# Kernel tuning notes

Measured on AMD Instinct MI355X. Metric: run time of the kernel, lower is better.

The kernel has to match this reference:

```python
import jax, jax.numpy as jnp
import numpy as np

B, S, D, H = 4, 2048, 2048, 16
Dh = D // H
BASE = 10000.0


def _rope_tables(seq_len, head_dim, dtype=jnp.float32):
    inv_freq = 1.0 / (BASE ** (jnp.arange(0, head_dim, 2, dtype=jnp.float32) / head_dim))
    t = jnp.arange(seq_len, dtype=jnp.float32)
    freqs = jnp.outer(t, inv_freq)              # [S, Dh/2]
    emb = jnp.concatenate([freqs, freqs], -1)   # [S, Dh]
    return jnp.cos(emb).astype(dtype), jnp.sin(emb).astype(dtype)


def _rotate_half(x):
    d = x.shape[-1] // 2
    return jnp.concatenate([-x[..., d:], x[..., :d]], axis=-1)


def setup_inputs() -> dict:
    key = jax.random.key(0)
    ks = jax.random.split(key, 5)
    std = D ** -0.5
    x = jax.random.normal(ks[0], (B, S, D), jnp.float32)
    Wq = jax.random.normal(ks[1], (D, D), jnp.float32) * std
    Wk = jax.random.normal(ks[2], (D, D), jnp.float32) * std
    Wv = jax.random.normal(ks[3], (D, D), jnp.float32) * std
    Wo = jax.random.normal(ks[4], (D, D), jnp.float32) * std
    attn_mask = jnp.triu(jnp.ones((S, S), dtype=bool), k=1)  # True = masked (causal)
    return {"x": x, "attn_mask": attn_mask, "Wq": Wq, "Wk": Wk, "Wv": Wv, "Wo": Wo}


def reference(x, attn_mask, Wq, Wk, Wv, Wo):
    b, s, d = x.shape
    # projections (nn.Linear: x @ W.T), split heads -> [B, H, S, Dh]
    q = (x @ Wq.T).reshape(b, s, H, Dh).transpose(0, 2, 1, 3)
    k = (x @ Wk.T).reshape(b, s, H, Dh).transpose(0, 2, 1, 3)
    v = (x @ Wv.T).reshape(b, s, H, Dh).transpose(0, 2, 1, 3)
    cos, sin = _rope_tables(s, Dh, x.dtype)     # [S, Dh]
    q = q * cos + _rotate_half(q) * sin
    k = k * cos + _rotate_half(k) * sin
    scale = Dh ** -0.5
    scores = jnp.einsum('bhqd,bhkd->bhqk', q, k) * scale
    scores = jnp.where(attn_mask[None, None, :, :], -jnp.inf, scores)
    weights = jax.nn.softmax(scores, axis=-1)
    out = jnp.einsum('bhqk,bhkd->bhqd', weights, v)
    out = out.transpose(0, 2, 1, 3).reshape(b, s, d)
    return out @ Wo.T
```

## Files before the change

kernel.cpp:

```cpp
#include <hip/hip_runtime.h>
#include <cstdint>
#include <cmath>

#define NB 4
#define NS 2048
#define ND 2048
#define NH 16
#define NDH 128
#define NM (NB*NS)

typedef unsigned short u16;
typedef __bf16 bf16x8 __attribute__((ext_vector_type(8)));
typedef u16    u16x8  __attribute__((ext_vector_type(8)));
typedef u16    u16x4  __attribute__((ext_vector_type(4)));
typedef float  f32x4  __attribute__((ext_vector_type(4)));
typedef float  f32x16 __attribute__((ext_vector_type(16)));
typedef unsigned u32x4_t __attribute__((ext_vector_type(4)));

__device__ __forceinline__ u16 f2bf(float f) {
  unsigned u = __float_as_uint(f);
  u += 0x7fffu + ((u >> 16) & 1u);
  return (u16)(u >> 16);
}
__device__ __forceinline__ float bf2f(u16 h) {
  return __uint_as_float(((unsigned)h) << 16);
}
__device__ __forceinline__ void gld16(const void* g, void* l) {
  __builtin_amdgcn_global_load_lds((__attribute__((address_space(1))) void*)g,
                                   (__attribute__((address_space(3))) void*)l,
                                   16, 0, 0);
}
__device__ __forceinline__ f32x4 mfma_bf16(bf16x8 a, bf16x8 b, f32x4 c) {
  return __builtin_amdgcn_mfma_f32_16x16x32_bf16(a, b, c, 0, 0, 0);
}
__device__ __forceinline__ f32x16 mfma32_bf16(bf16x8 a, bf16x8 b, f32x16 c) {
  return __builtin_amdgcn_mfma_f32_32x32x16_bf16(a, b, c, 0, 0, 0);
}
__device__ __forceinline__ unsigned cvtpk(float lo, float hi) {
  unsigned r;
  asm("v_cvt_pk_bf16_f32 %0, %1, %2" : "=v"(r) : "v"(lo), "v"(hi));
  return r;
}
__device__ __forceinline__ void p32swap(unsigned &a, unsigned &b) {
  asm volatile("v_permlane32_swap_b32 %0, %1" : "+v"(a), "+v"(b));
}

__global__ void cvt_bf16_kernel(const float* __restrict__ in, u16* __restrict__ out, int n8) {
  int i = blockIdx.x * 256 + threadIdx.x;
  if (i >= n8) return;
  const float4* p = (const float4*)in + (size_t)i * 2;
  float4 a = p[0], b = p[1];
  u16x8 r;
  r[0]=f2bf(a.x); r[1]=f2bf(a.y); r[2]=f2bf(a.z); r[3]=f2bf(a.w);
  r[4]=f2bf(b.x); r[5]=f2bf(b.y); r[6]=f2bf(b.z); r[7]=f2bf(b.w);
  ((u16x8*)out)[i] = r;
}

__global__ void cvt4_bf16_kernel(const float* __restrict__ i0, const float* __restrict__ i1,
                                 const float* __restrict__ i2, const float* __restrict__ i3,
                                 u16* o0, u16* o1, u16* o2, u16* o3, int n8each) {
  int idx = blockIdx.x * 256 + threadIdx.x;
  int w = idx / n8each, i = idx - w * n8each;
  if (w >= 4) return;
  const float* in = (w == 0) ? i0 : (w == 1) ? i1 : (w == 2) ? i2 : i3;
  u16* out = (w == 0) ? o0 : (w == 1) ? o1 : (w == 2) ? o2 : o3;
  const float4* p = (const float4*)in + (size_t)i * 2;
  float4 a = p[0], b = p[1];
  u16x8 r;
  r[0]=f2bf(a.x); r[1]=f2bf(a.y); r[2]=f2bf(a.z); r[3]=f2bf(a.w);
  r[4]=f2bf(b.x); r[5]=f2bf(b.y); r[6]=f2bf(b.z); r[7]=f2bf(b.w);
  ((u16x8*)out)[i] = r;
}

__global__ void rope_tables_kernel(float* __restrict__ cosT, float* __restrict__ sinT) {
  int s = blockIdx.x, d = threadIdx.x;
  double inv = pow(10000.0, -(double)d / 64.0);
  float ang = (float)((double)s * inv);
  cosT[s*64 + d] = cosf(ang);
  sinT[s*64 + d] = sinf(ang);
}

__global__ void rope_apply_kernel(u16* __restrict__ Qb, u16* __restrict__ Kb,
                                  const float* __restrict__ cosT,
                                  const float* __restrict__ sinT, int nthr) {
  int gidx = blockIdx.x * 256 + threadIdx.x;
  u16* X = (gidx < nthr) ? Qb : Kb;
  int idx = (gidx < nthr) ? gidx : gidx - nthr;
  int pc = idx & 7, h = (idx >> 3) & (NH - 1), m = idx >> 7;
  int s = m & (NS - 1);
  int d0 = pc * 8;
  size_t base = (size_t)m * ND + h * NDH + d0;
  u16x8 v0 = *(const u16x8*)(X + base);
  u16x8 v1 = *(const u16x8*)(X + base + 64);
  u16x8 r0, r1;
#pragma unroll
  for (int j = 0; j < 8; ++j) {
    float c  = cosT[s*64 + d0 + j];
    float sn = sinT[s*64 + d0 + j];
    float x0 = bf2f(v0[j]), x1 = bf2f(v1[j]);
    r0[j] = f2bf(x0 * c - x1 * sn);
    r1[j] = f2bf(x1 * c + x0 * sn);
  }
  *(u16x8*)(X + base)      = r0;
  *(u16x8*)(X + base + 64) = r1;
}

#define BARX do { __builtin_amdgcn_s_barrier(); __builtin_amdgcn_sched_barrier(0); } while (0)
#define VM4  do { asm volatile("s_waitcnt vmcnt(4)" ::: "memory"); \
                  __builtin_amdgcn_sched_barrier(0); } while (0)
#define GP(BUF, KS, MH, LOADB, WAITV, DOBAR, STAGE) do {                          \
  bf16x8 af[4];                                                                   \
  _Pragma("unroll")                                                               \
  for (int mf = 0; mf < 4; ++mf)                                                  \
    af[mf] = *(const bf16x8*)(Asb + (BUF)*32768 + (KS)*16384 + arow + ((MH)*4+mf)*1024); \
  if (LOADB) {                                                                    \
    _Pragma("unroll")                                                             \
    for (int nf = 0; nf < 4; ++nf)                                                \
      bfr[nf] = *(const bf16x8*)(Bsb + (BUF)*32768 + (KS)*16384 + brow + nf*1024); \
  }                                                                               \
  STAGE;                                                                          \
  __builtin_amdgcn_s_setprio(1);                                                  \
  _Pragma("unroll")                                                               \
  for (int mf = 0; mf < 4; ++mf)                                                  \
    _Pragma("unroll")                                                             \
    for (int nf = 0; nf < 4; ++nf)                                                \
      acc[(MH)*4+mf][nf] = mfma_bf16(af[mf], bfr[nf], acc[(MH)*4+mf][nf]);        \
  __builtin_amdgcn_s_setprio(0);                                                  \
  if (WAITV) VM4;                                                                 \
  if (DOBAR) BARX;                                                                \
} while (0)

template <typename OutT>
__global__ __launch_bounds__(512, 2) void gemm256_kernel(
    const u16* __restrict__ A,
    const u16* __restrict__ B0, const u16* __restrict__ B1, const u16* __restrict__ B2,
    OutT* __restrict__ C0, OutT* __restrict__ C1, OutT* __restrict__ C2,
    int Nd, int Kd) {
  __shared__ __align__(16) char Asb[65536];
  __shared__ __align__(16) char Bsb[65536];
  int tid = threadIdx.x;
  int wave = tid >> 6, lane = tid & 63;
  int li = lane & 15, lg = lane >> 4;
  int wr = wave >> 2, wc = wave & 3;
  int w  = (int)blockIdx.x >> 8;
  int tb = (int)blockIdx.x & 255;
  const u16* Bw = (w == 0) ? B0 : (w == 1) ? B1 : B2;
  OutT*      C  = (w == 0) ? C0 : (w == 1) ? C1 : C2;
  int NTn = Nd >> 8;
  int swz = (tb & 7) * 32 + (tb >> 3);
  int m0 = (swz / NTn) << 8, n0 = (swz % NTn) << 8;

  int rswz = (lg * 16) ^ (((li >> 1) & 3) << 4);
  int arow = (wr * 128 + li) * 64 + rswz;
  int brow = (wc *  64 + li) * 64 + rswz;

  int srow = wave * 16 + (lane >> 2);
  int scswz = ((lane & 3) * 16) ^ (((srow >> 1) & 3) << 4);
  size_t rowB = (size_t)Kd * 2;
  const char* Asrc = (const char*)A  + (size_t)(m0 + srow) * rowB + scswz;
  const char* Bsrc = (const char*)Bw + (size_t)(n0 + srow) * rowB + scswz;
  char* Adst = Asb + wave * 1024;
  char* Bdst = Bsb + wave * 1024;
  size_t half2 = rowB << 7;

  auto stageA = [&](int buf, int ks, int tile) {
    const char* s = Asrc + (size_t)tile * 128 + ks * 64;
    char* d = Adst + buf * 32768 + ks * 16384;
    gld16(s, d);
    gld16(s + half2, d + 8192);
  };
  auto stageB = [&](int buf, int ks, int tile) {
    const char* s = Bsrc + (size_t)tile * 128 + ks * 64;
    char* d = Bdst + buf * 32768 + ks * 16384;
    gld16(s, d);
    gld16(s + half2, d + 8192);
  };

  f32x4 acc[8][4] = {};
  bf16x8 bfr[4];

  int NKT = Kd >> 6;
  int NIT = NKT >> 1;

  stageA(0, 0, 0); stageA(0, 1, 0); stageB(0, 0, 0); stageB(0, 1, 0);
  stageA(1, 0, 1); stageB(1, 0, 1);
  asm volatile("s_waitcnt vmcnt(4)" ::: "memory");
  __builtin_amdgcn_sched_barrier(0);
  BARX;

  for (int j = 0; j < NIT; ++j) {
    int t1  = 2*j + 1;
    int tn0 = (2*j + 2) & (NKT - 1);
    int tn1 = (2*j + 3) & (NKT - 1);
    GP(0, 0, 0, true,  false, false, { stageA(1, 1, t1);  });
    GP(0, 0, 1, false, false, true,  { stageB(1, 1, t1);  });
    GP(0, 1, 1, true,  false, false, { stageA(0, 0, tn0); });
    GP(0, 1, 0, false, true,  true,  { stageB(0, 0, tn0); });
    GP(1, 0, 0, true,  false, false, { stageA(0, 1, tn0); });
    GP(1, 0, 1, false, false, true,  { stageB(0, 1, tn0); });
    GP(1, 1, 1, true,  false, false, { stageA(1, 0, tn1); });
    GP(1, 1, 0, false, true,  true,  { stageB(1, 0, tn1); });
  }
  asm volatile("s_waitcnt vmcnt(0)" ::: "memory");

  int rbase = m0 + wr*128 + lg*4;
  int cbase = n0 + wc*64 + li;
#pragma unroll
  for (int am = 0; am < 8; ++am)
#pragma unroll
    for (int nf = 0; nf < 4; ++nf)
#pragma unroll
      for (int r = 0; r < 4; ++r) {
        size_t off = (size_t)(rbase + am*16 + r) * Nd + (cbase + nf*16);
        if constexpr (sizeof(OutT) == 2) C[off] = f2bf(acc[am][nf][r]);
        else                             C[off] = acc[am][nf][r];
      }
}

__global__ __launch_bounds__(512, 2) void flash_attn_kernel(
    const u16* __restrict__ Q, const u16* __restrict__ K, const u16* __restrict__ V,
    u16* __restrict__ O) {
  __shared__ __align__(16) u16 Ks[2*64*128];
  __shared__ __align__(16) u16 Vt[2*128*64];
  int tid = threadIdx.x, wv = tid >> 6, lane = tid & 63;
  int ql = lane & 31, hi = lane >> 5;
  int b = blockIdx.x >> 4, h = blockIdx.x & 15;
  int qt = (int)gridDim.y - 1 - (int)blockIdx.y;
  int q0 = qt << 8;
  int qw = q0 + wv*32;
  int qa = qw + ql;
  int swzl = (ql & 7) << 4;
  int vswz = ((ql >> 1) & 7) << 4;
  const float qscale = 0.08838834764831845f * 1.4426950408889634f;

  bf16x8 qf[8];
  {
    const u16* qp = Q + (size_t)(b*NS + qa) * ND + h*NDH + hi*8;
#pragma unroll
    for (int ds = 0; ds < 8; ++ds) {
      u16x8 t = *(const u16x8*)(qp + ds*16);
      u16x8 r;
#pragma unroll
      for (int j = 0; j < 8; ++j) r[j] = f2bf(bf2f(t[j]) * qscale);
      qf[ds] = *(bf16x8*)&r;
    }
  }
  f32x16 o0 = {}, o1 = {}, o2 = {}, o3 = {};
  float m_run = -INFINITY, l_run = 0.f;

  const char* Kg = (const char*)(K + (size_t)b*NS*ND + h*NDH);
  const char* Vg = (const char*)(V + (size_t)b*NS*ND + h*NDH);
  const int ROWB = ND * 2;

  int p   = tid & 31;
  int kvg = tid >> 5;

  auto issueKV = [&](int kv0, int buf, unsigned (&dlo)[4], unsigned (&dhi)[4]) {
    const char* vrow = Vg + (size_t)(kv0 + kvg*4) * ROWB;
#pragma unroll
    for (int j = 0; j < 4; ++j) {
      dlo[j] = *(const unsigned*)(vrow + j*ROWB + p*4);
      dhi[j] = *(const unsigned*)(vrow + j*ROWB + 128 + p*4);
    }
    char* ksb = (char*)Ks + buf*16384;
#pragma unroll
    for (int c = 0; c < 2; ++c) {
      int s = c*8192 + wv*1024 + lane*16;
      int row = s >> 8;
      int within = (s & 255) ^ ((row & 7) << 4);
      gld16(Kg + (size_t)(kv0 + row)*ROWB + within, ksb + c*8192 + wv*1024);
    }
    __builtin_amdgcn_sched_barrier(0);
  };

  auto dostep = [&](int kv0, int buf, const unsigned (&dlo)[4], const unsigned (&dhi)[4],
                    bool hasNext) {
    if (hasNext) asm volatile("s_waitcnt vmcnt(10)" ::: "memory");
    else         asm volatile("s_waitcnt vmcnt(0)"  ::: "memory");
    __builtin_amdgcn_sched_barrier(0);
    __builtin_amdgcn_s_barrier();
    __builtin_amdgcn_sched_barrier(0);

    char* vtb = (char*)Vt + buf*16384;
    const char* ksb = (const char*)Ks + buf*16384;

    {
      u16x4 rA, rB, rC, rD;
#pragma unroll
      for (int j = 0; j < 4; ++j) {
        rA[j] = (u16)dlo[j]; rB[j] = (u16)(dlo[j] >> 16);
        rC[j] = (u16)dhi[j]; rD[j] = (u16)(dhi[j] >> 16);
      }
      int ws = (p & 7) << 4;
      int a0 = ((2*p   )*128 + kvg*8) ^ ws;
      int a1 = ((2*p+ 1)*128 + kvg*8) ^ ws;
      int a2 = ((2*p+64)*128 + kvg*8) ^ ws;
      int a3 = ((2*p+65)*128 + kvg*8) ^ ws;
      *(u16x4*)(vtb + a0) = rA;
      *(u16x4*)(vtb + a1) = rB;
      *(u16x4*)(vtb + a2) = rC;
      *(u16x4*)(vtb + a3) = rD;
    }

    f32x16 p0 = {}, p1 = {};
    __builtin_amdgcn_s_setprio(1);
#pragma unroll
    for (int ds = 0; ds < 8; ++ds) {
      bf16x8 kf0 = *(const bf16x8*)(ksb + ((ql*256 + ds*32 + hi*16) ^ swzl));
      p0 = mfma32_bf16(kf0, qf[ds], p0);
      bf16x8 kf1 = *(const bf16x8*)(ksb + (((32+ql)*256 + ds*32 + hi*16) ^ swzl));
      p1 = mfma32_bf16(kf1, qf[ds], p1);
    }
    __builtin_amdgcn_s_setprio(0);

    if (kv0 + 63 > qw) {
      int thresh = qa - kv0 - 4*hi;
#pragma unroll
      for (int r = 0; r < 16; ++r) {
        int c0 = (r & 3) + 8*(r >> 2);
        p0[r] = (c0      > thresh) ? -INFINITY : p0[r];
        p1[r] = (c0 + 32 > thresh) ? -INFINITY : p1[r];
      }
    }

    float mx[16];
#pragma unroll
    for (int r = 0; r < 16; ++r) mx[r] = fmaxf(p0[r], p1[r]);
#pragma unroll
    for (int s = 8; s > 0; s >>= 1)
#pragma unroll
      for (int r = 0; r < 8; ++r) if (r < s) mx[r] = fmaxf(mx[r], mx[r + s]);
    float pmax = fmaxf(mx[0], __shfl_xor(mx[0], 32, 64));

    if (!__all(pmax <= m_run + 8.f)) {
      float mn = fmaxf(m_run, pmax);
      float corr = __builtin_amdgcn_exp2f(m_run - mn);
      m_run = mn; l_run *= corr;
#pragma unroll
      for (int r = 0; r < 16; ++r) {
        float cw = __shfl(corr, (r & 3) + 8*(r >> 2) + 4*hi, 64);
        o0[r] *= cw; o1[r] *= cw; o2[r] *= cw; o3[r] *= cw;
      }
    }

    float sm[16];
#pragma unroll
    for (int r = 0; r < 16; ++r) {
      p0[r] = __builtin_amdgcn_exp2f(p0[r] - m_run);
      p1[r] = __builtin_amdgcn_exp2f(p1[r] - m_run);
      sm[r] = p0[r] + p1[r];
    }
#pragma unroll
    for (int s = 8; s > 0; s >>= 1)
#pragma unroll
      for (int r = 0; r < 8; ++r) if (r < s) sm[r] += sm[r + s];
    l_run += sm[0] + __shfl_xor(sm[0], 32, 64);

    bf16x8 pa0, pa1, pa2, pa3;
#define MKPA(P, B, OUT) {                              \
      unsigned a0 = cvtpk(P[(B)+0], P[(B)+1]);         \
      unsigned b0 = cvtpk(P[(B)+4], P[(B)+5]);         \
      p32swap(a0, b0);                                 \
      unsigned a1 = cvtpk(P[(B)+2], P[(B)+3]);         \
      unsigned b1 = cvtpk(P[(B)+6], P[(B)+7]);         \
      p32swap(a1, b1);                                 \
      u32x4_t w; w[0]=a0; w[1]=a1; w[2]=b0; w[3]=b1;   \
      OUT = *(bf16x8*)&w; }
    MKPA(p0, 0, pa0)
    MKPA(p0, 8, pa1)
    MKPA(p1, 0, pa2)
    MKPA(p1, 8, pa3)
#undef MKPA

    asm volatile("s_waitcnt lgkmcnt(0)" ::: "memory");
    __builtin_amdgcn_sched_barrier(0);
    __builtin_amdgcn_s_barrier();
    __builtin_amdgcn_sched_barrier(0);

    __builtin_amdgcn_s_setprio(1);
#define PVT(OT, T) {                                                        \
      _Pragma("unroll")                                                     \
      for (int ks = 0; ks < 4; ++ks) {                                      \
        int a = ((((T)*32 + ql)*128 + ks*32 + hi*16) ^ vswz);               \
        bf16x8 vf = *(const bf16x8*)(vtb + a);                              \
        OT = mfma32_bf16(ks==0?pa0:ks==1?pa1:ks==2?pa2:pa3, vf, OT);        \
      } }
    PVT(o0, 0)
    PVT(o1, 1)
    PVT(o2, 2)
    PVT(o3, 3)
#undef PVT
    __builtin_amdgcn_s_setprio(0);
  };

  int nt = 4*qt + 4;
  unsigned dloA[4], dhiA[4], dloB[4], dhiB[4];
  issueKV(0, 0, dloA, dhiA);
  for (int t = 0; ; t += 2) {
    bool h1 = (t+1 < nt);
    if (h1) issueKV((t+1)*64, 1, dloB, dhiB);
    dostep(t*64, 0, dloA, dhiA, h1);
    if (!h1) break;
    bool h2 = (t+2 < nt);
    if (h2) issueKV((t+2)*64, 0, dloA, dhiA);
    dostep((t+1)*64, 1, dloB, dhiB, h2);
    if (!h2) break;
  }

  float inv = 1.0f / l_run;
#pragma unroll
  for (int r = 0; r < 16; ++r) {
    int crow = (r & 3) + 8*(r >> 2) + 4*hi;
    float iv = __shfl(inv, crow, 64);
    size_t base = (size_t)(b*NS + qw + crow) * ND + h*NDH + ql;
    O[base +  0] = f2bf(o0[r] * iv);
    O[base + 32] = f2bf(o1[r] * iv);
    O[base + 64] = f2bf(o2[r] * iv);
    O[base + 96] = f2bf(o3[r] * iv);
  }
}

extern "C" void kernel_launch(void* const* d_in, const int* in_sizes, int n_in,
                              void* d_out, int out_size, void* d_ws, size_t ws_size,
                              hipStream_t stream) {
  const float* x  = (const float*)d_in[0];
  const float* Wq = (const float*)d_in[2];
  const float* Wk = (const float*)d_in[3];
  const float* Wv = (const float*)d_in[4];
  const float* Wo = (const float*)d_in[5];

  char* ws = (char*)d_ws;
  const size_t SZ_MD = (size_t)NM * ND * 2;
  const size_t SZ_W  = (size_t)ND * ND * 2;
  u16* xb  = (u16*)(ws);
  u16* Qb  = (u16*)(ws + SZ_MD);
  u16* Kb  = (u16*)(ws + 2*SZ_MD);
  u16* Vb  = (u16*)(ws + 3*SZ_MD);
  u16* Ab  = (u16*)(ws + 4*SZ_MD);
  u16* Wqb = (u16*)(ws + 5*SZ_MD);
  u16* Wkb = (u16*)(ws + 5*SZ_MD + SZ_W);
  u16* Wvb = (u16*)(ws + 5*SZ_MD + 2*SZ_W);
  u16* Wob = (u16*)(ws + 5*SZ_MD + 3*SZ_W);
  float* cosT = (float*)(ws + 5*SZ_MD + 4*SZ_W);
  float* sinT = (float*)(ws + 5*SZ_MD + 4*SZ_W + (size_t)NS*64*4);
  size_t needed = 5*SZ_MD + 4*SZ_W + 2*(size_t)NS*64*4;
  if (ws_size < needed) return;

  {
    int n8 = (NM * ND) / 8;
    cvt_bf16_kernel<<<(n8 + 255)/256, 256, 0, stream>>>(x, xb, n8);
    int w8 = (ND * ND) / 8;
    cvt4_bf16_kernel<<<(4*w8 + 255)/256, 256, 0, stream>>>(Wq, Wk, Wv, Wo,
                                                           Wqb, Wkb, Wvb, Wob, w8);
  }
  rope_tables_kernel<<<NS, 64, 0, stream>>>(cosT, sinT);

  gemm256_kernel<u16><<<3*256, 512, 0, stream>>>(xb, Wqb, Wkb, Wvb,
                                                 Qb, Kb, Vb, ND, ND);

  {
    int nthr = NM * NH * 8;
    rope_apply_kernel<<<(2*nthr)/256, 256, 0, stream>>>(Qb, Kb, cosT, sinT, nthr);
  }

  flash_attn_kernel<<<dim3(NB*NH, NS/256), 512, 0, stream>>>(Qb, Kb, Vb, Ab);

  gemm256_kernel<float><<<256, 512, 0, stream>>>(Ab, Wob, nullptr, nullptr,
                                                 (float*)d_out, nullptr, nullptr, ND, ND);
}
```

Baseline: 413.4 us.

## Pair long and short causal query tiles per block to share K/V loads

Each flash-attention block now handles two query tiles, a late one (4+y) and an early one (3-y), so every block does the same amount of causal work. Each K/V tile staged in LDS is used by both query sets. The grid shrinks from 8 to 4 tiles along y. This is meant to remove causal load imbalance and halve K/V traffic, but it doubles the accumulator and Q-fragment registers, which risks spilling or lower occupancy under launch_bounds(512,2), and halves the block count.

```diff
diff --git a/kernel.cpp b/kernel.cpp
--- a/kernel.cpp
+++ b/kernel.cpp
@@ -44,6 +44,16 @@
 __device__ __forceinline__ void p32swap(unsigned &a, unsigned &b) {
   asm volatile("v_permlane32_swap_b32 %0, %1" : "+v"(a), "+v"(b));
 }
+
+#define MKPA(P, B, OUT) {                              \
+      unsigned a0 = cvtpk(P[(B)+0], P[(B)+1]);         \
+      unsigned b0 = cvtpk(P[(B)+4], P[(B)+5]);         \
+      p32swap(a0, b0);                                 \
+      unsigned a1 = cvtpk(P[(B)+2], P[(B)+3]);         \
+      unsigned b1 = cvtpk(P[(B)+6], P[(B)+7]);         \
+      p32swap(a1, b1);                                 \
+      u32x4_t w_; w_[0]=a0; w_[1]=a1; w_[2]=b0; w_[3]=b1; \
+      OUT = *(bf16x8*)&w_; }
 
 __global__ void cvt_bf16_kernel(const float* __restrict__ in, u16* __restrict__ out, int n8) {
   int i = blockIdx.x * 256 + threadIdx.x;
@@ -217,6 +227,79 @@
       }
 }
 
+#define QKSM(SUF) do {                                                         \
+    f32x16 p0 = {}, p1 = {};                                                   \
+    __builtin_amdgcn_s_setprio(1);                                             \
+    _Pragma("unroll")                                                          \
+    for (int ds = 0; ds < 8; ++ds) {                                           \
+      bf16x8 kf0 = *(const bf16x8*)(ksb + ((ql*256 + ds*32 + hi*16) ^ swzl));  \
+      p0 = mfma32_bf16(kf0, qf##SUF[ds], p0);                                  \
+      bf16x8 kf1 = *(const bf16x8*)(ksb + (((32+ql)*256 + ds*32 + hi*16) ^ swzl)); \
+      p1 = mfma32_bf16(kf1, qf##SUF[ds], p1);                                  \
+    }                                                                          \
+    __builtin_amdgcn_s_setprio(0);                                             \
+    if (kv0 + 63 > qw##SUF) {                                                  \
+      int thresh = qa##SUF - kv0 - 4*hi;                                       \
+      _Pragma("unroll")                                                        \
+      for (int r = 0; r < 16; ++r) {                                           \
+        int c0 = (r & 3) + 8*(r >> 2);                                         \
+        p0[r] = (c0      > thresh) ? -INFINITY : p0[r];                        \
+        p1[r] = (c0 + 32 > thresh) ? -INFINITY : p1[r];                        \
+      }                                                                        \
+    }                                                                          \
+    float mx[16];                                                              \
+    _Pragma("unroll")                                                          \
+    for (int r = 0; r < 16; ++r) mx[r] = fmaxf(p0[r], p1[r]);                  \
+    _Pragma("unroll")                                                          \
+    for (int s_ = 8; s_ > 0; s_ >>= 1)                                         \
+      _Pragma("unroll")                                                        \
+      for (int r = 0; r < 8; ++r) if (r < s_) mx[r] = fmaxf(mx[r], mx[r + s_]); \
+    float pmax = fmaxf(mx[0], __shfl_xor(mx[0], 32, 64));                      \
+    if (!__all(pmax <= m##SUF + 8.f)) {                                        \
+      float mn = fmaxf(m##SUF, pmax);                                          \
+      float corr = __builtin_amdgcn_exp2f(m##SUF - mn);                        \
+      m##SUF = mn; l##SUF *= corr;                                             \
+      _Pragma("unroll")                                                        \
+      for (int r = 0; r < 16; ++r) {                                           \
+        float cw = __shfl(corr, (r & 3) + 8*(r >> 2) + 4*hi, 64);              \
+        o##SUF##0[r] *= cw; o##SUF##1[r] *= cw;                                \
+        o##SUF##2[r] *= cw; o##SUF##3[r] *= cw;                                \
+      }                                                                        \
+    }                                                                          \
+    float sm[16];                                                              \
+    _Pragma("unroll")                                                          \
+    for (int r = 0; r < 16; ++r) {                                             \
+      p0[r] = __builtin_amdgcn_exp2f(p0[r] - m##SUF);                          \
+      p1[r] = __builtin_amdgcn_exp2f(p1[r] - m##SUF);                          \
+      sm[r] = p0[r] + p1[r];                                                   \
+    }                                                                          \
+    _Pragma("unroll")                                                          \
+    for (int s_ = 8; s_ > 0; s_ >>= 1)                                         \
+      _Pragma("unroll")                                                        \
+      for (int r = 0; r < 8; ++r) if (r < s_) sm[r] += sm[r + s_];             \
+    l##SUF += sm[0] + __shfl_xor(sm[0], 32, 64);                               \
+    MKPA(p0, 0, pa##SUF##0)                                                    \
+    MKPA(p0, 8, pa##SUF##1)                                                    \
+    MKPA(p1, 0, pa##SUF##2)                                                    \
+    MKPA(p1, 8, pa##SUF##3)                                                    \
+  } while (0)
+
+#define PVT1(OT, T, P0, P1, P2, P3)                                            \
+    _Pragma("unroll")                                                          \
+    for (int ks_ = 0; ks_ < 4; ++ks_) {                                        \
+      int a_ = ((((T)*32 + ql)*128 + ks_*32 + hi*16) ^ vswz);                  \
+      bf16x8 vf = *(const bf16x8*)(vtb + a_);                                  \
+      OT = mfma32_bf16(ks_==0?P0:ks_==1?P1:ks_==2?P2:P3, vf, OT);              \
+    }
+#define PVS(SUF) do {                                                          \
+    __builtin_amdgcn_s_setprio(1);                                             \
+    PVT1(o##SUF##0, 0, pa##SUF##0, pa##SUF##1, pa##SUF##2, pa##SUF##3)         \
+    PVT1(o##SUF##1, 1, pa##SUF##0, pa##SUF##1, pa##SUF##2, pa##SUF##3)         \
+    PVT1(o##SUF##2, 2, pa##SUF##0, pa##SUF##1, pa##SUF##2, pa##SUF##3)         \
+    PVT1(o##SUF##3, 3, pa##SUF##0, pa##SUF##1, pa##SUF##2, pa##SUF##3)         \
+    __builtin_amdgcn_s_setprio(0);                                             \
+  } while (0)
+
 __global__ __launch_bounds__(512, 2) void flash_attn_kernel(
     const u16* __restrict__ Q, const u16* __restrict__ K, const u16* __restrict__ V,
     u16* __restrict__ O) {
@@ -225,28 +308,37 @@
   int tid = threadIdx.x, wv = tid >> 6, lane = tid & 63;
   int ql = lane & 31, hi = lane >> 5;
   int b = blockIdx.x >> 4, h = blockIdx.x & 15;
-  int qt = (int)gridDim.y - 1 - (int)blockIdx.y;
-  int q0 = qt << 8;
-  int qw = q0 + wv*32;
-  int qa = qw + ql;
+  int y = blockIdx.y;
+  int qtA = 4 + y, qtB = 3 - y;
+  int q0A = qtA << 8, q0B = qtB << 8;
+  int qwA = q0A + wv*32, qwB = q0B + wv*32;
+  int qaA = qwA + ql,  qaB = qwB + ql;
   int swzl = (ql & 7) << 4;
   int vswz = ((ql >> 1) & 7) << 4;
   const float qscale = 0.08838834764831845f * 1.4426950408889634f;
 
-  bf16x8 qf[8];
+  bf16x8 qfA[8], qfB[8];
   {
-    const u16* qp = Q + (size_t)(b*NS + qa) * ND + h*NDH + hi*8;
+    const u16* qpA = Q + (size_t)(b*NS + qaA) * ND + h*NDH + hi*8;
+    const u16* qpB = Q + (size_t)(b*NS + qaB) * ND + h*NDH + hi*8;
 #pragma unroll
     for (int ds = 0; ds < 8; ++ds) {
-      u16x8 t = *(const u16x8*)(qp + ds*16);
-      u16x8 r;
-#pragma unroll
-      for (int j = 0; j < 8; ++j) r[j] = f2bf(bf2f(t[j]) * qscale);
-      qf[ds] = *(bf16x8*)&r;
+      u16x8 tA = *(const u16x8*)(qpA + ds*16);
+      u16x8 tB = *(const u16x8*)(qpB + ds*16);
+      u16x8 rA, rB;
+#pragma unroll
+      for (int j = 0; j < 8; ++j) {
+        rA[j] = f2bf(bf2f(tA[j]) * qscale);
+        rB[j] = f2bf(bf2f(tB[j]) * qscale);
+      }
+      qfA[ds] = *(bf16x8*)&rA;
+      qfB[ds] = *(bf16x8*)&rB;
     }
   }
-  f32x16 o0 = {}, o1 = {}, o2 = {}, o3 = {};
-  float m_run = -INFINITY, l_run = 0.f;
+  f32x16 oA0 = {}, oA1 = {}, oA2 = {}, oA3 = {};
+  f32x16 oB0 = {}, oB1 = {}, oB2 = {}, oB3 = {};
+  float mA = -INFINITY, lA = 0.f, mB = -INFINITY, lB = 0.f;
+  bf16x8 paA0, paA1, paA2, paA3, paB0, paB1, paB2, paB3;
 
   const char* Kg = (const char*)(K + (size_t)b*NS*ND + h*NDH);
   const char* Vg = (const char*)(V + (size_t)b*NS*ND + h*NDH);
@@ -292,131 +384,55 @@
         rC[j] = (u16)dhi[j]; rD[j] = (u16)(dhi[j] >> 16);
       }
       int ws = (p & 7) << 4;
-      int a0 = ((2*p   )*128 + kvg*8) ^ ws;
-      int a1 = ((2*p+ 1)*128 + kvg*8) ^ ws;
-      int a2 = ((2*p+64)*128 + kvg*8) ^ ws;
-      int a3 = ((2*p+65)*128 + kvg*8) ^ ws;
-      *(u16x4*)(vtb + a0) = rA;
-      *(u16x4*)(vtb + a1) = rB;
-      *(u16x4*)(vtb + a2) = rC;
-      *(u16x4*)(vtb + a3) = rD;
+      *(u16x4*)(vtb + (((2*p   )*128 + kvg*8) ^ ws)) = rA;
+      *(u16x4*)(vtb + (((2*p+ 1)*128 + kvg*8) ^ ws)) = rB;
+      *(u16x4*)(vtb + (((2*p+64)*128 + kvg*8) ^ ws)) = rC;
+      *(u16x4*)(vtb + (((2*p+65)*128 + kvg*8) ^ ws)) = rD;
     }
 
-    f32x16 p0 = {}, p1 = {};
-    __builtin_amdgcn_s_setprio(1);
-#pragma unroll
-    for (int ds = 0; ds < 8; ++ds) {
-      bf16x8 kf0 = *(const bf16x8*)(ksb + ((ql*256 + ds*32 + hi*16) ^ swzl));
-      p0 = mfma32_bf16(kf0, qf[ds], p0);
-      bf16x8 kf1 = *(const bf16x8*)(ksb + (((32+ql)*256 + ds*32 + hi*16) ^ swzl));
-      p1 = mfma32_bf16(kf1, qf[ds], p1);
-    }
-    __builtin_amdgcn_s_setprio(0);
-
-    if (kv0 + 63 > qw) {
-      int thresh = qa - kv0 - 4*hi;
-#pragma unroll
-      for (int r = 0; r < 16; ++r) {
-        int c0 = (r & 3) + 8*(r >> 2);
-        p0[r] = (c0      > thresh) ? -INFINITY : p0[r];
-        p1[r] = (c0 + 32 > thresh) ? -INFINITY : p1[r];
-      }
-    }
-
-    float mx[16];
-#pragma unroll
-    for (int r = 0; r < 16; ++r) mx[r] = fmaxf(p0[r], p1[r]);
-#pragma unroll
-    for (int s = 8; s > 0; s >>= 1)
-#pragma unroll
-      for (int r = 0; r < 8; ++r) if (r < s) mx[r] = fmaxf(mx[r], mx[r + s]);
-    float pmax = fmaxf(mx[0], __shfl_xor(mx[0], 32, 64));
-
-    if (!__all(pmax <= m_run + 8.f)) {
-      float mn = fmaxf(m_run, pmax);
-      float corr = __builtin_amdgcn_exp2f(m_run - mn);
-      m_run = mn; l_run *= corr;
-#pragma unroll
-      for (int r = 0; r < 16; ++r) {
-        float cw = __shfl(corr, (r & 3) + 8*(r >> 2) + 4*hi, 64);
-        o0[r] *= cw; o1[r] *= cw; o2[r] *= cw; o3[r] *= cw;
-      }
-    }
-
-    float sm[16];
-#pragma unroll
-    for (int r = 0; r < 16; ++r) {
-      p0[r] = __builtin_amdgcn_exp2f(p0[r] - m_run);
-      p1[r] = __builtin_amdgcn_exp2f(p1[r] - m_run);
-      sm[r] = p0[r] + p1[r];
-    }
-#pragma unroll
-    for (int s = 8; s > 0; s >>= 1)
-#pragma unroll
-      for (int r = 0; r < 8; ++r) if (r < s) sm[r] += sm[r + s];
-    l_run += sm[0] + __shfl_xor(sm[0], 32, 64);
-
-    bf16x8 pa0, pa1, pa2, pa3;
-#define MKPA(P, B, OUT) {                              \
-      unsigned a0 = cvtpk(P[(B)+0], P[(B)+1]);         \
-      unsigned b0 = cvtpk(P[(B)+4], P[(B)+5]);         \
-      p32swap(a0, b0);                                 \
-      unsigned a1 = cvtpk(P[(B)+2], P[(B)+3]);         \
-      unsigned b1 = cvtpk(P[(B)+6], P[(B)+7]);         \
-      p32swap(a1, b1);                                 \
-      u32x4_t w; w[0]=a0; w[1]=a1; w[2]=b0; w[3]=b1;   \
-      OUT = *(bf16x8*)&w; }
-    MKPA(p0, 0, pa0)
-    MKPA(p0, 8, pa1)
-    MKPA(p1, 0, pa2)
-    MKPA(p1, 8, pa3)
-#undef MKPA
+    bool doB = kv0 < q0B + 256;
+    QKSM(A);
+    if (doB) QKSM(B);
 
     asm volatile("s_waitcnt lgkmcnt(0)" ::: "memory");
     __builtin_amdgcn_sched_barrier(0);
     __builtin_amdgcn_s_barrier();
     __builtin_amdgcn_sched_barrier(0);
 
-    __builtin_amdgcn_s_setprio(1);
-#define PVT(OT, T) {                                                        \
-      _Pragma("unroll")                                                     \
-      for (int ks = 0; ks < 4; ++ks) {                                      \
-        int a = ((((T)*32 + ql)*128 + ks*32 + hi*16) ^ vswz);               \
-        bf16x8 vf = *(const bf16x8*)(vtb + a);                              \
-        OT = mfma32_bf16(ks==0?pa0:ks==1?pa1:ks==2?pa2:pa3, vf, OT);        \
-      } }
-    PVT(o0, 0)
-    PVT(o1, 1)
-    PVT(o2, 2)
-    PVT(o3, 3)
-#undef PVT
-    __builtin_amdgcn_s_setprio(0);
+    PVS(A);
+    if (doB) PVS(B);
   };
 
-  int nt = 4*qt + 4;
-  unsigned dloA[4], dhiA[4], dloB[4], dhiB[4];
-  issueKV(0, 0, dloA, dhiA);
+  int nt = 4*qtA + 4;
+  unsigned dloA_[4], dhiA_[4], dloB_[4], dhiB_[4];
+  issueKV(0, 0, dloA_, dhiA_);
   for (int t = 0; ; t += 2) {
     bool h1 = (t+1 < nt);
-    if (h1) issueKV((t+1)*64, 1, dloB, dhiB);
-    dostep(t*64, 0, dloA, dhiA, h1);
+    if (h1) issueKV((t+1)*64, 1, dloB_, dhiB_);
+    dostep(t*64, 0, dloA_, dhiA_, h1);
     if (!h1) break;
     bool h2 = (t+2 < nt);
-    if (h2) issueKV((t+2)*64, 0, dloA, dhiA);
-    dostep((t+1)*64, 1, dloB, dhiB, h2);
+    if (h2) issueKV((t+2)*64, 0, dloA_, dhiA_);
+    dostep((t+1)*64, 1, dloB_, dhiB_, h2);
     if (!h2) break;
   }
 
-  float inv = 1.0f / l_run;
+  float invA = 1.0f / lA, invB = 1.0f / lB;
 #pragma unroll
   for (int r = 0; r < 16; ++r) {
     int crow = (r & 3) + 8*(r >> 2) + 4*hi;
-    float iv = __shfl(inv, crow, 64);
-    size_t base = (size_t)(b*NS + qw + crow) * ND + h*NDH + ql;
-    O[base +  0] = f2bf(o0[r] * iv);
-    O[base + 32] = f2bf(o1[r] * iv);
-    O[base + 64] = f2bf(o2[r] * iv);
-    O[base + 96] = f2bf(o3[r] * iv);
+    float ivA = __shfl(invA, crow, 64);
+    float ivB = __shfl(invB, crow, 64);
+    size_t baseA = (size_t)(b*NS + qwA + crow) * ND + h*NDH + ql;
+    size_t baseB = (size_t)(b*NS + qwB + crow) * ND + h*NDH + ql;
+    O[baseA +  0] = f2bf(oA0[r] * ivA);
+    O[baseA + 32] = f2bf(oA1[r] * ivA);
+    O[baseA + 64] = f2bf(oA2[r] * ivA);
+    O[baseA + 96] = f2bf(oA3[r] * ivA);
+    O[baseB +  0] = f2bf(oB0[r] * ivB);
+    O[baseB + 32] = f2bf(oB1[r] * ivB);
+    O[baseB + 64] = f2bf(oB2[r] * ivB);
+    O[baseB + 96] = f2bf(oB3[r] * ivB);
   }
 }
 
@@ -463,7 +479,7 @@
     rope_apply_kernel<<<(2*nthr)/256, 256, 0, stream>>>(Qb, Kb, cosT, sinT, nthr);
   }
 
-  flash_attn_kernel<<<dim3(NB*NH, NS/256), 512, 0, stream>>>(Qb, Kb, Vb, Ab);
+  flash_attn_kernel<<<dim3(NB*NH, 4), 512, 0, stream>>>(Qb, Kb, Vb, Ab);
 
   gemm256_kernel<float><<<256, 512, 0, stream>>>(Ab, Wob, nullptr, nullptr,
                                                  (float*)d_out, nullptr, nullptr, ND, ND);
```

Measured after the change: 721.4 us. 74.5% more time.
